# Optimization experiments

Measured on AMD Instinct MI355X. Metric: run time of the kernel, lower is better.

Reference implementation:

```python
import jax, jax.numpy as jnp
import numpy as np

B, T, C, A, P = 16, 1024, 512, 4096, 256  # batch, frames, phones, allophone arcs, phonemes


def setup_inputs() -> dict:
    key = jax.random.key(0)
    k1, k2, k3 = jax.random.split(key, 3)
    hs_pad = jax.random.normal(k1, (B, T, C), dtype=jnp.float32)
    # each phone has exactly A // C allophone arcs (full coverage, balanced)
    phone_arc_labels = jnp.arange(A, dtype=jnp.int32) % C
    arcs_per_phone = A // C
    # weights near -log(arcs_per_phone) so sum_a exp(log_prob + w) ~= 1,
    # matching a trained allophone layer and keeping the redis step log-safe
    alloW = 0.01 * jax.random.normal(k2, (A,), dtype=jnp.float32) - jnp.log(
        jnp.float32(arcs_per_phone)
    )
    phoneme_arc_labels = jax.random.randint(k3, (A,), 0, P, dtype=jnp.int32)
    return {
        "hs_pad": hs_pad,
        "alloW": alloW,
        "phone_arc_labels": phone_arc_labels,
        "phoneme_arc_labels": phoneme_arc_labels,
        "n_phonemes": P,
    }


def reference(hs_pad, alloW, phone_arc_labels, phoneme_arc_labels, n_phonemes):
    # log_softmax over phones
    log_probs = jax.nn.log_softmax(hs_pad, axis=-1)  # [B,T,C]
    # WFST intersection of linear emission graph with 1-state allophone graph:
    # arc a gets weight log_probs[..., phone_label(a)] + alloW[a]
    new_emissions = log_probs[..., phone_arc_labels] + alloW  # [B,T,A]
    # squash many phones per phoneme: exp + scatter-add over output labels
    ex = jnp.exp(new_emissions)
    Bq, Tq = ex.shape[0], ex.shape[1]
    squashed = jnp.zeros((Bq, Tq, n_phonemes), dtype=ex.dtype)
    squashed = squashed.at[..., phoneme_arc_labels].add(ex)  # [B,T,P]
    # redistribute probability mass so it sums to 1
    redistributed = (squashed.sum(axis=-1) - 1.0)[..., None] / n_phonemes
    squashed = squashed - redistributed
    return jnp.log(squashed)
```

## Files before the change

### kernel.cpp

```cpp
#include <hip/hip_runtime.h>
#include <hip/hip_bf16.h>

#define BT   16384
#define CDIM 512
#define ADIM 4096
#define PDIM 256

typedef __attribute__((ext_vector_type(8))) short short8;
typedef __attribute__((ext_vector_type(4))) float f32x4;

__device__ __forceinline__ unsigned short bf16_rne(float f) {
    unsigned int u = __float_as_uint(f);
    u += 0x7FFFu + ((u >> 16) & 1u);
    return (unsigned short)(u >> 16);
}

__global__ __launch_bounds__(256) void build_Wf(const float* __restrict__ alloW,
                                                const int* __restrict__ phone_lab,
                                                const int* __restrict__ phoneme_lab,
                                                unsigned short* __restrict__ Wf) {
    __shared__ float wrow[PDIM];
    const int c = blockIdx.x;
    const int t = threadIdx.x;
    wrow[t] = 0.0f;
    __syncthreads();
#pragma unroll
    for (int i = 0; i < ADIM / 256; ++i) {
        int a = i * 256 + t;
        if (phone_lab[a] == c)
            atomicAdd(&wrow[phoneme_lab[a]], __expf(alloW[a]));
    }
    __syncthreads();
    const int slot = (t & ~31) | ((t & 1) << 4) | ((t & 31) >> 1);
    Wf[(c >> 5) * (PDIM * 32) + slot * 32 + (c & 31)] = bf16_rne(wrow[t]);
}

__global__ __launch_bounds__(512, 4) void allo_fused(const float* __restrict__ hs,
                                                     const unsigned short* __restrict__ Wf,
                                                     float* __restrict__ out) {
    __shared__ __align__(16) unsigned short Af[2 * 16 * 16 * 32];
    __shared__ float invZ[32];
    __shared__ float psum[8][32];

    const int tid  = threadIdx.x;
    const int row0 = blockIdx.x * 32;

    const int wave = tid >> 6;
    const int lane = tid & 63;
    const int c    = lane & 15;
    const int q    = lane >> 4;

    const unsigned short* wb  = Wf + (size_t)(wave * 32 + c) * 32 + q * 8;
    const unsigned short* af0 = Af + c * 32 + q * 8;

    short8 nb0 = *(const short8*)(wb);
    short8 nb1 = *(const short8*)(wb + 512);

    {
        const int r   = tid >> 4;
        const int ksl = tid & 15;
        const int rb  = r >> 4;
        const int cc  = r & 15;
        const float* hsr = hs + (size_t)(row0 + r) * CDIM + ksl * 4;
        unsigned short* af = Af + rb * 8192 + (ksl >> 3) * 512 + cc * 32 + (ksl & 7) * 4;

        float s = 0.0f;
#pragma unroll
        for (int i = 0; i < 8; ++i) {
            float4 v = *(const float4*)(hsr + i * 64);
            float e0 = __expf(v.x), e1 = __expf(v.y);
            float e2 = __expf(v.z), e3 = __expf(v.w);
            s += (e0 + e1) + (e2 + e3);
            ushort4 pk;
            pk.x = bf16_rne(e0); pk.y = bf16_rne(e1);
            pk.z = bf16_rne(e2); pk.w = bf16_rne(e3);
            *(ushort4*)(af + i * 1024) = pk;
        }
        s += __shfl_xor(s, 1);
        s += __shfl_xor(s, 2);
        s += __shfl_xor(s, 4);
        s += __shfl_xor(s, 8);
        if (ksl == 0) invZ[r] = 1.0f / s;
    }
    __syncthreads();

    f32x4 acc[2][2];
#pragma unroll
    for (int rb = 0; rb < 2; ++rb)
#pragma unroll
        for (int cb = 0; cb < 2; ++cb)
            acc[rb][cb] = (f32x4){0.f, 0.f, 0.f, 0.f};

#pragma unroll
    for (int kb = 0; kb < 16; ++kb) {
        short8 b0 = nb0;
        short8 b1 = nb1;
        if (kb < 15) {
            const unsigned short* wkb = wb + (kb + 1) * 8192;
            nb0 = *(const short8*)(wkb);
            nb1 = *(const short8*)(wkb + 512);
        }
        short8 a0 = *(const short8*)(af0 + kb * 512);
        short8 a1 = *(const short8*)(af0 + 8192 + kb * 512);

        acc[0][0] = __builtin_amdgcn_mfma_f32_16x16x32_bf16(a0, b0, acc[0][0], 0, 0, 0);
        acc[0][1] = __builtin_amdgcn_mfma_f32_16x16x32_bf16(a0, b1, acc[0][1], 0, 0, 0);
        acc[1][0] = __builtin_amdgcn_mfma_f32_16x16x32_bf16(a1, b0, acc[1][0], 0, 0, 0);
        acc[1][1] = __builtin_amdgcn_mfma_f32_16x16x32_bf16(a1, b1, acc[1][1], 0, 0, 0);
    }

    float sp[2][4];
#pragma unroll
    for (int rb = 0; rb < 2; ++rb)
#pragma unroll
        for (int r = 0; r < 4; ++r) {
            float v = acc[rb][0][r] + acc[rb][1][r];
            v += __shfl_xor(v, 1);
            v += __shfl_xor(v, 2);
            v += __shfl_xor(v, 4);
            v += __shfl_xor(v, 8);
            sp[rb][r] = v;
        }
    if (c == 0) {
#pragma unroll
        for (int rb = 0; rb < 2; ++rb)
#pragma unroll
            for (int r = 0; r < 4; ++r)
                psum[wave][rb * 16 + q * 4 + r] = sp[rb][r];
    }
    __syncthreads();

#pragma unroll
    for (int rb = 0; rb < 2; ++rb)
#pragma unroll
        for (int r = 0; r < 4; ++r) {
            const int rr  = rb * 16 + q * 4 + r;
            const float iz = invZ[rr];
            float Ssum = 0.0f;
#pragma unroll
            for (int w = 0; w < 8; ++w) Ssum += psum[w][rr];
            const float S    = Ssum * iz;
            const float corr = (S - 1.0f) * (1.0f / (float)PDIM);
            float2 o;
            o.x = __logf(acc[rb][0][r] * iz - corr);
            o.y = __logf(acc[rb][1][r] * iz - corr);
            *(float2*)(out + (size_t)(row0 + rr) * PDIM + wave * 32 + 2 * c) = o;
        }
}

extern "C" void kernel_launch(void* const* d_in, const int* in_sizes, int n_in,
                              void* d_out, int out_size, void* d_ws, size_t ws_size,
                              hipStream_t stream) {
    const float* hs          = (const float*)d_in[0];
    const float* alloW       = (const float*)d_in[1];
    const int*   phone_lab   = (const int*)d_in[2];
    const int*   phoneme_lab = (const int*)d_in[3];
    float*       out         = (float*)d_out;

    unsigned short* Wf = (unsigned short*)d_ws;

    build_Wf<<<CDIM, 256, 0, stream>>>(alloW, phone_lab, phoneme_lab, Wf);
    allo_fused<<<BT / 32, 512, 0, stream>>>(hs, Wf, out);
}
```

Measured before the change: 100.5 us.

## Fuse weight-matrix construction into main kernel via per-block LDS scatter

Drops the separate build_Wf kernel. Each block now rebuilds the phone-to-phoneme weight slice for every k-block in shared memory, using LDS atomics into a swizzled float buffer, and converts it to bf16 before the MFMA. This removes one kernel launch and the global weight buffer. In exchange, all 512 blocks repeat the scatter work, the main loop gains three barriers per k-step plus atomics, and the extra 32KB of LDS may lower occupancy.

```diff
diff --git a/kernel.cpp b/kernel.cpp
--- a/kernel.cpp
+++ b/kernel.cpp
@@ -1,5 +1,4 @@
 #include <hip/hip_runtime.h>
-#include <hip/hip_bf16.h>
 
 #define BT   16384
 #define CDIM 512
@@ -15,46 +14,36 @@
     return (unsigned short)(u >> 16);
 }
 
-__global__ __launch_bounds__(256) void build_Wf(const float* __restrict__ alloW,
-                                                const int* __restrict__ phone_lab,
-                                                const int* __restrict__ phoneme_lab,
-                                                unsigned short* __restrict__ Wf) {
-    __shared__ float wrow[PDIM];
-    const int c = blockIdx.x;
-    const int t = threadIdx.x;
-    wrow[t] = 0.0f;
-    __syncthreads();
-#pragma unroll
-    for (int i = 0; i < ADIM / 256; ++i) {
-        int a = i * 256 + t;
-        if (phone_lab[a] == c)
-            atomicAdd(&wrow[phoneme_lab[a]], __expf(alloW[a]));
-    }
-    __syncthreads();
-    const int slot = (t & ~31) | ((t & 1) << 4) | ((t & 31) >> 1);
-    Wf[(c >> 5) * (PDIM * 32) + slot * 32 + (c & 31)] = bf16_rne(wrow[t]);
-}
-
-__global__ __launch_bounds__(512, 4) void allo_fused(const float* __restrict__ hs,
-                                                     const unsigned short* __restrict__ Wf,
-                                                     float* __restrict__ out) {
+__global__ __launch_bounds__(512, 4) void allo_all(const float* __restrict__ hs,
+                                                   const float* __restrict__ alloW,
+                                                   const int* __restrict__ phone_lab,
+                                                   const int* __restrict__ phoneme_lab,
+                                                   float* __restrict__ out) {
     __shared__ __align__(16) unsigned short Af[2 * 16 * 16 * 32];
+    __shared__ __align__(16) float Wacc[8192];
     __shared__ float invZ[32];
     __shared__ float psum[8][32];
 
     const int tid  = threadIdx.x;
     const int row0 = blockIdx.x * 32;
-
     const int wave = tid >> 6;
     const int lane = tid & 63;
     const int c    = lane & 15;
     const int q    = lane >> 4;
 
-    const unsigned short* wb  = Wf + (size_t)(wave * 32 + c) * 32 + q * 8;
-    const unsigned short* af0 = Af + c * 32 + q * 8;
-
-    short8 nb0 = *(const short8*)(wb);
-    short8 nb1 = *(const short8*)(wb + 512);
+    float ew[8];
+    int   widx[8];
+    int   pkb[8];
+#pragma unroll
+    for (int i = 0; i < 8; ++i) {
+        const int a  = i * 512 + tid;
+        const int ph = phone_lab[a];
+        const int p  = phoneme_lab[a];
+        ew[i]  = __expf(alloW[a]);
+        pkb[i] = ph >> 5;
+        const int slot = (p & ~31) | ((p & 1) << 4) | ((p & 31) >> 1);
+        widx[i] = (slot * 32 + (ph & 31)) ^ ((slot & 7) << 2);
+    }
 
     {
         const int r   = tid >> 4;
@@ -82,7 +71,15 @@
         s += __shfl_xor(s, 8);
         if (ksl == 0) invZ[r] = 1.0f / s;
     }
-    __syncthreads();
+
+    const int S0 = wave * 32 + c;
+    const int sw = (S0 & 7) << 4;
+    const float* wa00 = Wacc + ((((S0)      * 128 + q * 32 +  0) ^ sw) >> 2);
+    const float* wa01 = Wacc + ((((S0)      * 128 + q * 32 + 16) ^ sw) >> 2);
+    const float* wa10 = Wacc + ((((S0 + 16) * 128 + q * 32 +  0) ^ sw) >> 2);
+    const float* wa11 = Wacc + ((((S0 + 16) * 128 + q * 32 + 16) ^ sw) >> 2);
+    const unsigned short* af0 = Af + c * 32 + q * 8;
+    float4* W4 = (float4*)Wacc;
 
     f32x4 acc[2][2];
 #pragma unroll
@@ -91,15 +88,31 @@
         for (int cb = 0; cb < 2; ++cb)
             acc[rb][cb] = (f32x4){0.f, 0.f, 0.f, 0.f};
 
+    for (int kb = 0; kb < 16; ++kb) {
+        __syncthreads();
+        const float4 z4 = {0.f, 0.f, 0.f, 0.f};
 #pragma unroll
-    for (int kb = 0; kb < 16; ++kb) {
-        short8 b0 = nb0;
-        short8 b1 = nb1;
-        if (kb < 15) {
-            const unsigned short* wkb = wb + (kb + 1) * 8192;
-            nb0 = *(const short8*)(wkb);
-            nb1 = *(const short8*)(wkb + 512);
-        }
+        for (int j = 0; j < 4; ++j) W4[tid + j * 512] = z4;
+        __syncthreads();
+#pragma unroll
+        for (int i = 0; i < 8; ++i)
+            if (pkb[i] == kb) atomicAdd(&Wacc[widx[i]], ew[i]);
+        __syncthreads();
+
+        float4 f00 = *(const float4*)wa00;
+        float4 f01 = *(const float4*)wa01;
+        float4 f10 = *(const float4*)wa10;
+        float4 f11 = *(const float4*)wa11;
+        short8 b0, b1;
+        b0[0] = (short)bf16_rne(f00.x); b0[1] = (short)bf16_rne(f00.y);
+        b0[2] = (short)bf16_rne(f00.z); b0[3] = (short)bf16_rne(f00.w);
+        b0[4] = (short)bf16_rne(f01.x); b0[5] = (short)bf16_rne(f01.y);
+        b0[6] = (short)bf16_rne(f01.z); b0[7] = (short)bf16_rne(f01.w);
+        b1[0] = (short)bf16_rne(f10.x); b1[1] = (short)bf16_rne(f10.y);
+        b1[2] = (short)bf16_rne(f10.z); b1[3] = (short)bf16_rne(f10.w);
+        b1[4] = (short)bf16_rne(f11.x); b1[5] = (short)bf16_rne(f11.y);
+        b1[6] = (short)bf16_rne(f11.z); b1[7] = (short)bf16_rne(f11.w);
+
         short8 a0 = *(const short8*)(af0 + kb * 512);
         short8 a1 = *(const short8*)(af0 + 8192 + kb * 512);
 
@@ -157,8 +170,7 @@
     const int*   phoneme_lab = (const int*)d_in[3];
     float*       out         = (float*)d_out;
 
-    unsigned short* Wf = (unsigned short*)d_ws;
+    (void)d_ws; (void)ws_size;
 
-    build_Wf<<<CDIM, 256, 0, stream>>>(alloW, phone_lab, phoneme_lab, Wf);
-    allo_fused<<<BT / 32, 512, 0, stream>>>(hs, Wf, out);
+    allo_all<<<BT / 32, 512, 0, stream>>>(hs, alloW, phone_lab, phoneme_lab, out);
 }
```

New measurement: 112.3 us. 11.8% more time.
